# Kernel tuning notes

Hardware: AMD Instinct MI355X
Metric: run time of the kernel (lower is better)

## Reference

```python
import jax, jax.numpy as jnp
import numpy as np

P = 16           # patch size
E = P * P        # embed dim of MHA (must equal dim)
NH = 4           # num heads
HD = E // NH     # head dim


def setup_inputs() -> dict:
    key = jax.random.key(0)
    k1, k2, k3, k4, k5 = jax.random.split(key, 5)
    B, C, H, W = 2, 256, 256, 256
    scale = 1.0 / np.sqrt(E)
    return {
        "x": jax.random.normal(k1, (B, C, H, W), dtype=jnp.float32),
        "w_in": jax.random.normal(k2, (3 * E, E), dtype=jnp.float32) * scale,
        "b_in": jnp.zeros((3 * E,), dtype=jnp.float32),
        "w_out": jax.random.normal(k3, (E, E), dtype=jnp.float32) * scale,
        "b_out": jnp.zeros((E,), dtype=jnp.float32),
    }


def reference(x, w_in, b_in, w_out, b_out):
    B, C, H, W = x.shape
    nP = (H // P) * (W // P)
    # x.unfold(2,p,p).unfold(3,p,p).reshape(B,C,-1,p*p)
    patches = (
        x.reshape(B, C, H // P, P, W // P, P)
        .transpose(0, 1, 2, 4, 3, 5)
        .reshape(B, C, nP, E)
    )
    # permute(0,2,1,3).reshape(B*nP, C, p*p): batch=B*nP, seq=C, embed=E
    t = patches.transpose(0, 2, 1, 3).reshape(B * nP, C, E)

    qkv = t @ w_in.T + b_in                      # (N, C, 3E)
    q, k, v = jnp.split(qkv, 3, axis=-1)

    def to_heads(a):  # (N, C, E) -> (N, NH, C, HD)
        return a.reshape(B * nP, C, NH, HD).transpose(0, 2, 1, 3)

    q, k, v = to_heads(q), to_heads(k), to_heads(v)
    scores = jnp.einsum("nhqd,nhkd->nhqk", q * (HD ** -0.5), k)
    attn = jax.nn.softmax(scores, axis=-1)
    o = jnp.einsum("nhqk,nhkd->nhqd", attn, v)   # (N, NH, C, HD)
    o = o.transpose(0, 2, 1, 3).reshape(B * nP, C, E)
    o = o @ w_out.T + b_out
    # reshape(B, -1, C, p*p).permute(0, 2, 1, 3)
    return o.reshape(B, nP, C, E).transpose(0, 2, 1, 3)
```

## Files before the change

### kernel.cpp

```cpp
#include <hip/hip_runtime.h>
#include <hip/hip_bf16.h>

typedef __attribute__((ext_vector_type(8))) short s16x8;
typedef __attribute__((ext_vector_type(4))) float f32x4;

#define WS_SEG 67108864ULL

#if defined(__has_attribute)
#if __has_attribute(amdgpu_num_vgpr)
#define VGPR_CAP_128 __attribute__((amdgpu_num_vgpr(128)))
#else
#define VGPR_CAP_128
#endif
#else
#define VGPR_CAP_128
#endif

static __device__ __forceinline__ unsigned short f2bf(float f) {
    return __builtin_bit_cast(unsigned short, __float2bfloat16(f));
}
static __device__ __forceinline__ unsigned int pack2(float a, float b) {
    return (unsigned int)f2bf(a) | ((unsigned int)f2bf(b) << 16);
}
static __device__ __forceinline__ s16x8 u4cast(uint4 u) {
    return __builtin_bit_cast(s16x8, u);
}
static __device__ __forceinline__ void gl_lds16(const void* g, void* l) {
    __builtin_amdgcn_global_load_lds(
        (const __attribute__((address_space(1))) unsigned int*)g,
        (__attribute__((address_space(3))) unsigned int*)l, 16, 0, 0);
}

__global__ __launch_bounds__(256) void convw_swz(const float* __restrict__ wi,
                                                 unsigned short* __restrict__ wb) {
    int i = (blockIdx.x * 256 + threadIdx.x) * 4;
    float4 v = *reinterpret_cast<const float4*>(wi + i);
    int bb = i * 2;
    int row = i >> 8;
    int dst = (bb & ~127) | ((bb & 127) ^ ((row & 7) << 4));
    uint2 o = { pack2(v.x, v.y), pack2(v.z, v.w) };
    *reinterpret_cast<uint2*>((char*)wb + dst) = o;
}

__global__ __launch_bounds__(256) void gather_swz(const float* __restrict__ x,
                                                  unsigned short* __restrict__ t) {
    int q = (blockIdx.x * 256 + threadIdx.x) * 4;
    int e = q & 255, c = (q >> 8) & 255, n = q >> 16;
    int b = n >> 8, p = n & 255;
    int xi = ((b * 256 + c) * 256 + (p >> 4) * 16 + (e >> 4)) * 256 + (p & 15) * 16 + (e & 15);
    float4 v = *reinterpret_cast<const float4*>(x + xi);
    int bb = q * 2;
    int row = q >> 8;
    int dst = (bb & ~127) | ((bb & 127) ^ ((row & 7) << 4));
    uint2 o = { pack2(v.x, v.y), pack2(v.z, v.w) };
    *reinterpret_cast<uint2*>((char*)t + dst) = o;
}

template<int MODE>
__global__ __launch_bounds__(256) void gemm8(
    const unsigned short* __restrict__ Ab,
    const unsigned short* __restrict__ Wb,
    const float* __restrict__ bias,
    unsigned short* __restrict__ Qo, unsigned short* __restrict__ Ko,
    unsigned short* __restrict__ Vt, float* __restrict__ Out)
{
    __shared__ __align__(16) char smem[65536];
    char* AsB = smem;
    char* BsB = smem + 32768;

    const int t = threadIdx.x, w = t >> 6, lane = t & 63;
    const int lr = lane & 15, lk = lane >> 4;
    const int wm = w >> 1, wn = w & 1;

    constexpr int NB = (MODE == 0) ? 6 : 2;
    const int flat = blockIdx.x;
    const int xcd = flat & 7, idx = flat >> 3;
    const int bm = xcd * 128 + idx / NB;
    const int bn = idx % NB;

    const char* Ag = (const char*)Ab + (size_t)bm * 65536;
    const char* Bg = (const char*)Wb + (size_t)bn * 65536;

    const bool swapped = (MODE == 1) || (bn < 4);

    auto stage = [&](int kk) {
        char* Ad = AsB + (kk & 1) * 16384;
        char* Bd = BsB + (kk & 1) * 16384;
        #pragma unroll
        for (int i = 0; i < 4; ++i) {
            int u = (i * 4 + w) * 64 + lane;
            int row = u >> 3, cb = (u & 7) * 16;
            gl_lds16(Ag + row * 512 + kk * 128 + cb, Ad + (i * 4 + w) * 1024);
            gl_lds16(Bg + row * 512 + kk * 128 + cb, Bd + (i * 4 + w) * 1024);
        }
    };

    f32x4 acc[4][4] = {};

    stage(0);
    for (int kk = 0; kk < 4; ++kk) {
        __syncthreads();
        if (kk < 3) stage(kk + 1);
        const char* Ac = AsB + (kk & 1) * 16384;
        const char* Bc = BsB + (kk & 1) * 16384;
        #pragma unroll
        for (int kc = 0; kc < 2; ++kc) {
            s16x8 af[4], bf[4];
            #pragma unroll
            for (int fm = 0; fm < 4; ++fm) {
                int r = wm * 64 + fm * 16 + lr;
                af[fm] = *reinterpret_cast<const s16x8*>(
                    Ac + r * 128 + ((kc * 64 + lk * 16) ^ ((r & 7) << 4)));
            }
            #pragma unroll
            for (int fn = 0; fn < 4; ++fn) {
                int cc = wn * 64 + fn * 16 + lr;
                bf[fn] = *reinterpret_cast<const s16x8*>(
                    Bc + cc * 128 + ((kc * 64 + lk * 16) ^ ((cc & 7) << 4)));
            }
            if (swapped) {
                #pragma unroll
                for (int fm = 0; fm < 4; ++fm)
                    #pragma unroll
                    for (int fn = 0; fn < 4; ++fn)
                        acc[fm][fn] = __builtin_amdgcn_mfma_f32_16x16x32_bf16(bf[fn], af[fm], acc[fm][fn], 0, 0, 0);
            } else {
                #pragma unroll
                for (int fm = 0; fm < 4; ++fm)
                    #pragma unroll
                    for (int fn = 0; fn < 4; ++fn)
                        acc[fm][fn] = __builtin_amdgcn_mfma_f32_16x16x32_bf16(af[fm], bf[fn], acc[fm][fn], 0, 0, 0);
            }
        }
    }

    const int n = bm >> 1;

    if (MODE == 0) {
        if (bn < 4) {
            unsigned short* base = (bn >> 1) ? Ko : Qo;
            const int h0 = (bn & 1) * 2;
            const float qs = (bn >> 1) ? 1.0f : 0.18033688011112042f;
            #pragma unroll
            for (int fn = 0; fn < 4; ++fn) {
                int col_local = wn * 64 + fn * 16 + lk * 4;
                f32x4 bv4 = *reinterpret_cast<const f32x4*>(bias + bn * 128 + col_local);
                int h = h0 + (col_local >> 6), d0 = col_local & 63;
                #pragma unroll
                for (int fm = 0; fm < 4; ++fm) {
                    int c = (bm & 1) * 128 + wm * 64 + fm * 16 + lr;
                    uint2 st = { pack2((acc[fm][fn][0] + bv4[0]) * qs, (acc[fm][fn][1] + bv4[1]) * qs),
                                 pack2((acc[fm][fn][2] + bv4[2]) * qs, (acc[fm][fn][3] + bv4[3]) * qs) };
                    *reinterpret_cast<uint2*>(
                        (char*)base + (size_t)((n * 4 + h) * 256 + c) * 128 + d0 * 2) = st;
                }
            }
        } else {
            const int h0 = (bn - 4) * 2;
            #pragma unroll
            for (int fn = 0; fn < 4; ++fn) {
                int col_local = wn * 64 + fn * 16 + lr;
                float bv = bias[bn * 128 + col_local];
                int hl = col_local >> 6, d = col_local & 63;
                #pragma unroll
                for (int fm = 0; fm < 4; ++fm) {
                    int c = (bm & 1) * 128 + wm * 64 + fm * 16 + lk * 4;
                    uint2 st = { pack2(acc[fm][fn][0] + bv, acc[fm][fn][1] + bv),
                                 pack2(acc[fm][fn][2] + bv, acc[fm][fn][3] + bv) };
                    *reinterpret_cast<uint2*>(
                        (char*)Vt + (size_t)((n * 4 + h0 + hl) * 64 + d) * 512 + c * 2) = st;
                }
            }
        }
    } else {
        #pragma unroll
        for (int fn = 0; fn < 4; ++fn) {
            int colg = bn * 128 + wn * 64 + fn * 16 + lk * 4;
            f32x4 bv4 = *reinterpret_cast<const f32x4*>(bias + colg);
            #pragma unroll
            for (int fm = 0; fm < 4; ++fm) {
                int rg = bm * 128 + wm * 64 + fm * 16 + lr;
                int nn = rg >> 8, c = rg & 255;
                int b = nn >> 8, p = nn & 255;
                f32x4 st = acc[fm][fn] + bv4;
                *reinterpret_cast<f32x4*>(
                    Out + (((size_t)(b * 256 + c) * 256 + p) << 8) + colg) = st;
            }
        }
    }
}

__global__ __launch_bounds__(1024) VGPR_CAP_128 void attn8(
    const unsigned short* __restrict__ Q,
    const unsigned short* __restrict__ K,
    const unsigned short* __restrict__ V,
    unsigned short* __restrict__ O)
{
    __shared__ __align__(16) char KsB[32768];
    __shared__ __align__(16) char VsB[32768];

    const int nh = blockIdx.x;
    const int n = nh >> 2, h = nh & 3;
    const int t = threadIdx.x, w = t >> 6, lane = t & 63;
    const int lr = lane & 15, lk = lane >> 4;

    const unsigned short* Qg = Q + (size_t)nh * 16384;
    const char* Kg = (const char*)K + (size_t)nh * 32768;
    const char* Vg = (const char*)V + (size_t)nh * 32768;

    #pragma unroll
    for (int i = 0; i < 2; ++i) {
        int u = i * 1024 + t;
        int row = u >> 3, cb = (u & 7) * 16;
        uint4 val = *reinterpret_cast<const uint4*>(Kg + u * 16);
        *reinterpret_cast<uint4*>(KsB + row * 128 + (cb ^ ((row & 7) << 4))) = val;
    }
    #pragma unroll
    for (int i = 0; i < 2; ++i) {
        int u = i * 1024 + t;
        int row = u >> 5, cb = (u & 31) * 16;
        uint4 val = *reinterpret_cast<const uint4*>(Vg + u * 16);
        *reinterpret_cast<uint4*>(VsB + row * 512 + (cb ^ ((row & 7) << 4))) = val;
    }
    __syncthreads();

    const int swz = (lr & 7) << 4;
    const int qt = w;

    s16x8 bq0 = *reinterpret_cast<const s16x8*>(Qg + (qt * 16 + lr) * 64 + lk * 8);
    s16x8 bq1 = *reinterpret_cast<const s16x8*>(Qg + (qt * 16 + lr) * 64 + 32 + lk * 8);

    f32x4 oacc[4] = {};
    float l = 0.f;

    #pragma unroll
    for (int kb = 0; kb < 8; ++kb) {
        const int rb0 = ((2 * kb) * 16 + lr) * 128;
        const int rb1 = ((2 * kb + 1) * 16 + lr) * 128;
        s16x8 a00 = *reinterpret_cast<const s16x8*>(KsB + rb0 + ((lk * 16) ^ swz));
        s16x8 a01 = *reinterpret_cast<const s16x8*>(KsB + rb0 + ((64 + lk * 16) ^ swz));
        s16x8 a10 = *reinterpret_cast<const s16x8*>(KsB + rb1 + ((lk * 16) ^ swz));
        s16x8 a11 = *reinterpret_cast<const s16x8*>(KsB + rb1 + ((64 + lk * 16) ^ swz));
        f32x4 s0 = { 0.f, 0.f, 0.f, 0.f }, s1 = { 0.f, 0.f, 0.f, 0.f };
        __builtin_amdgcn_s_setprio(1);
        s0 = __builtin_amdgcn_mfma_f32_16x16x32_bf16(a00, bq0, s0, 0, 0, 0);
        s0 = __builtin_amdgcn_mfma_f32_16x16x32_bf16(a01, bq1, s0, 0, 0, 0);
        s1 = __builtin_amdgcn_mfma_f32_16x16x32_bf16(a10, bq0, s1, 0, 0, 0);
        s1 = __builtin_amdgcn_mfma_f32_16x16x32_bf16(a11, bq1, s1, 0, 0, 0);
        __builtin_amdgcn_s_setprio(0);

        float p0 = exp2f(s0[0]), p1 = exp2f(s0[1]);
        float p2 = exp2f(s0[2]), p3 = exp2f(s0[3]);
        float p4 = exp2f(s1[0]), p5 = exp2f(s1[1]);
        float p6 = exp2f(s1[2]), p7 = exp2f(s1[3]);
        l += ((p0 + p1) + (p2 + p3)) + ((p4 + p5) + (p6 + p7));
        uint4 pk = { pack2(p0, p1), pack2(p2, p3), pack2(p4, p5), pack2(p6, p7) };
        s16x8 pf = u4cast(pk);

        __builtin_amdgcn_s_setprio(1);
        #pragma unroll
        for (int dt = 0; dt < 4; ++dt) {
            const char* vb = VsB + (dt * 16 + lr) * 512;
            uint2 v0 = *reinterpret_cast<const uint2*>(vb + ((kb * 64 + lk * 8) ^ swz));
            uint2 v1 = *reinterpret_cast<const uint2*>(vb + ((kb * 64 + lk * 8 + 32) ^ swz));
            uint4 uu = { v0.x, v0.y, v1.x, v1.y };
            oacc[dt] = __builtin_amdgcn_mfma_f32_16x16x32_bf16(u4cast(uu), pf, oacc[dt], 0, 0, 0);
        }
        __builtin_amdgcn_s_setprio(0);
    }

    l += __shfl_xor(l, 16);
    l += __shfl_xor(l, 32);
    const float rl = 1.0f / l;

    char* orow = (char*)O + (size_t)(n * 256 + qt * 16 + lr) * 512 + h * 128;
    #pragma unroll
    for (int dt = 0; dt < 4; ++dt) {
        uint2 st = { pack2(oacc[dt][0] * rl, oacc[dt][1] * rl),
                     pack2(oacc[dt][2] * rl, oacc[dt][3] * rl) };
        *reinterpret_cast<uint2*>(orow + ((dt * 32 + lk * 8) ^ swz)) = st;
    }
}

extern "C" void kernel_launch(void* const* d_in, const int* in_sizes, int n_in,
                              void* d_out, int out_size, void* d_ws, size_t ws_size,
                              hipStream_t stream) {
    const float* x     = (const float*)d_in[0];
    const float* w_in  = (const float*)d_in[1];
    const float* b_in  = (const float*)d_in[2];
    const float* w_out = (const float*)d_in[3];
    const float* b_out = (const float*)d_in[4];

    char* ws = (char*)d_ws;
    unsigned short* tO = (unsigned short*)(ws);
    unsigned short* Qw = (unsigned short*)(ws + WS_SEG);
    unsigned short* Kw = (unsigned short*)(ws + 2 * WS_SEG);
    unsigned short* Vw = (unsigned short*)(ws + 3 * WS_SEG);

    unsigned short* WbIn = (unsigned short*)((float*)d_out + out_size - 98304);

    convw_swz<<<192, 256, 0, stream>>>(w_in, WbIn);
    gather_swz<<<32768, 256, 0, stream>>>(x, tO);

    gemm8<0><<<6144, 256, 0, stream>>>(tO, WbIn, b_in, Qw, Kw, Vw, nullptr);

    attn8<<<2048, 1024, 0, stream>>>(Qw, Kw, Vw, tO);

    unsigned short* WbOut = Kw;
    convw_swz<<<64, 256, 0, stream>>>(w_out, WbOut);

    gemm8<1><<<2048, 256, 0, stream>>>(tO, WbOut, b_out,
                                       nullptr, nullptr, nullptr, (float*)d_out);
}
```

Baseline: 289.2 us.

## Fuse patch gather into QKV projection GEMM with fragment-packed weights

```diff
diff --git a/kernel.cpp b/kernel.cpp
--- a/kernel.cpp
+++ b/kernel.cpp
@@ -31,6 +31,21 @@
         (__attribute__((address_space(3))) unsigned int*)l, 16, 0, 0);
 }
 
+__global__ __launch_bounds__(256) void convw_frag(const float* __restrict__ wi,
+                                                  unsigned short* __restrict__ wp) {
+    int o8 = blockIdx.x * 256 + threadIdx.x;
+    int nkc = o8 >> 10;
+    int rem = o8 & 1023;
+    int row = rem >> 2;
+    int lk8 = (rem & 3) * 8;
+    int Ni = nkc >> 3, kk = (nkc >> 1) & 3, kc = nkc & 1;
+    const float* src = wi + ((size_t)(Ni * 256 + row)) * 256 + kk * 64 + kc * 32 + lk8;
+    float4 a = *reinterpret_cast<const float4*>(src);
+    float4 b = *reinterpret_cast<const float4*>(src + 4);
+    uint4 o = { pack2(a.x, a.y), pack2(a.z, a.w), pack2(b.x, b.y), pack2(b.z, b.w) };
+    *reinterpret_cast<uint4*>(wp + o8 * 8) = o;
+}
+
 __global__ __launch_bounds__(256) void convw_swz(const float* __restrict__ wi,
                                                  unsigned short* __restrict__ wb) {
     int i = (blockIdx.x * 256 + threadIdx.x) * 4;
@@ -42,27 +57,126 @@
     *reinterpret_cast<uint2*>((char*)wb + dst) = o;
 }
 
-__global__ __launch_bounds__(256) void gather_swz(const float* __restrict__ x,
-                                                  unsigned short* __restrict__ t) {
-    int q = (blockIdx.x * 256 + threadIdx.x) * 4;
-    int e = q & 255, c = (q >> 8) & 255, n = q >> 16;
-    int b = n >> 8, p = n & 255;
-    int xi = ((b * 256 + c) * 256 + (p >> 4) * 16 + (e >> 4)) * 256 + (p & 15) * 16 + (e & 15);
-    float4 v = *reinterpret_cast<const float4*>(x + xi);
-    int bb = q * 2;
-    int row = q >> 8;
-    int dst = (bb & ~127) | ((bb & 127) ^ ((row & 7) << 4));
-    uint2 o = { pack2(v.x, v.y), pack2(v.z, v.w) };
-    *reinterpret_cast<uint2*>((char*)t + dst) = o;
-}
-
-template<int MODE>
-__global__ __launch_bounds__(256) void gemm8(
+__global__ __launch_bounds__(512) void qkv_fused(
+    const float* __restrict__ Xf,
+    const unsigned short* __restrict__ Wp,
+    const float* __restrict__ bias,
+    unsigned short* __restrict__ Qo, unsigned short* __restrict__ Ko,
+    unsigned short* __restrict__ Vt)
+{
+    __shared__ __align__(16) char AsB[131072];
+
+    const int t = threadIdx.x, w = t >> 6, lane = t & 63;
+    const int lr = lane & 15, lk = lane >> 4;
+    const int wm = w >> 2, wn = w & 3;
+
+    const int bid = blockIdx.x;
+    const int b = bid >> 8, pp = (bid >> 1) & 127, ch = bid & 1;
+    const int p16 = pp >> 3, col0 = (pp & 7) * 32;
+    const int c0 = ch * 128;
+
+    {
+        const float* xb = Xf + ((size_t)(b * 256 + c0) * 256 + p16 * 16) * 256 + col0;
+        #pragma unroll
+        for (int j = 0; j < 16; ++j) {
+            int u = j * 512 + t;
+            int c = u >> 6;
+            int r = (u >> 2) & 15;
+            int cf8 = (u & 3) * 8;
+            const float* p = xb + ((size_t)c * 256 + r) * 256 + cf8;
+            float4 a = *reinterpret_cast<const float4*>(p);
+            float4 b4 = *reinterpret_cast<const float4*>(p + 4);
+            int m = ((cf8 >> 4) << 7) + c;
+            int within = (r & 3) * 32 + (cf8 & 15) * 2;
+            int addr = m * 512 + (r >> 2) * 128 + (within ^ ((m & 7) << 4));
+            uint4 o = { pack2(a.x, a.y), pack2(a.z, a.w),
+                        pack2(b4.x, b4.y), pack2(b4.z, b4.w) };
+            *reinterpret_cast<uint4*>(AsB + addr) = o;
+        }
+    }
+    __syncthreads();
+
+    const int n = b * 256 + pp * 2 + wm;
+
+    #pragma unroll
+    for (int Ni = 0; Ni < 3; ++Ni) {
+        f32x4 acc[8][4] = {};
+        #pragma unroll
+        for (int kk = 0; kk < 4; ++kk) {
+            #pragma unroll
+            for (int kc = 0; kc < 2; ++kc) {
+                const char* wbase = (const char*)Wp + (((Ni * 4 + kk) * 2 + kc) << 14);
+                s16x8 bfr[4];
+                #pragma unroll
+                for (int fn = 0; fn < 4; ++fn)
+                    bfr[fn] = *reinterpret_cast<const s16x8*>(
+                        wbase + ((wn * 64 + fn * 16 + lr) * 32 + lk * 8) * 2);
+                const int e2 = kk * 128 + kc * 64 + lk * 16;
+                const int cbase = e2 & ~127, within = e2 & 127;
+                s16x8 afr[8];
+                #pragma unroll
+                for (int fm = 0; fm < 8; ++fm) {
+                    int m = wm * 128 + fm * 16 + lr;
+                    afr[fm] = *reinterpret_cast<const s16x8*>(
+                        AsB + m * 512 + cbase + (within ^ ((m & 7) << 4)));
+                }
+                if (Ni < 2) {
+                    #pragma unroll
+                    for (int fm = 0; fm < 8; ++fm)
+                        #pragma unroll
+                        for (int fn = 0; fn < 4; ++fn)
+                            acc[fm][fn] = __builtin_amdgcn_mfma_f32_16x16x32_bf16(bfr[fn], afr[fm], acc[fm][fn], 0, 0, 0);
+                } else {
+                    #pragma unroll
+                    for (int fm = 0; fm < 8; ++fm)
+                        #pragma unroll
+                        for (int fn = 0; fn < 4; ++fn)
+                            acc[fm][fn] = __builtin_amdgcn_mfma_f32_16x16x32_bf16(afr[fm], bfr[fn], acc[fm][fn], 0, 0, 0);
+                }
+            }
+        }
+
+        if (Ni < 2) {
+            unsigned short* base = Ni ? Ko : Qo;
+            const float qs = Ni ? 1.0f : 0.18033688011112042f;
+            #pragma unroll
+            for (int fn = 0; fn < 4; ++fn) {
+                int colq = wn * 64 + fn * 16 + lk * 4;
+                f32x4 bv4 = *reinterpret_cast<const f32x4*>(bias + Ni * 256 + colq);
+                int h = colq >> 6, d0 = colq & 63;
+                #pragma unroll
+                for (int fm = 0; fm < 8; ++fm) {
+                    int c = c0 + fm * 16 + lr;
+                    uint2 st = { pack2((acc[fm][fn][0] + bv4[0]) * qs, (acc[fm][fn][1] + bv4[1]) * qs),
+                                 pack2((acc[fm][fn][2] + bv4[2]) * qs, (acc[fm][fn][3] + bv4[3]) * qs) };
+                    *reinterpret_cast<uint2*>(
+                        (char*)base + (size_t)((n * 4 + h) * 256 + c) * 128 + d0 * 2) = st;
+                }
+            }
+        } else {
+            #pragma unroll
+            for (int fn = 0; fn < 4; ++fn) {
+                int dcol = wn * 64 + fn * 16 + lr;
+                float bv = bias[512 + dcol];
+                int h = dcol >> 6, d = dcol & 63;
+                #pragma unroll
+                for (int fm = 0; fm < 8; ++fm) {
+                    int c = c0 + fm * 16 + lk * 4;
+                    uint2 st = { pack2(acc[fm][fn][0] + bv, acc[fm][fn][1] + bv),
+                                 pack2(acc[fm][fn][2] + bv, acc[fm][fn][3] + bv) };
+                    *reinterpret_cast<uint2*>(
+                        (char*)Vt + (size_t)((n * 4 + h) * 64 + d) * 512 + c * 2) = st;
+                }
+            }
+        }
+    }
+}
+
+__global__ __launch_bounds__(256) void gemm_out(
     const unsigned short* __restrict__ Ab,
     const unsigned short* __restrict__ Wb,
     const float* __restrict__ bias,
-    unsigned short* __restrict__ Qo, unsigned short* __restrict__ Ko,
-    unsigned short* __restrict__ Vt, float* __restrict__ Out)
+    float* __restrict__ Out)
 {
     __shared__ __align__(16) char smem[65536];
     char* AsB = smem;
@@ -72,16 +186,13 @@
     const int lr = lane & 15, lk = lane >> 4;
     const int wm = w >> 1, wn = w & 1;
 
-    constexpr int NB = (MODE == 0) ? 6 : 2;
     const int flat = blockIdx.x;
     const int xcd = flat & 7, idx = flat >> 3;
-    const int bm = xcd * 128 + idx / NB;
-    const int bn = idx % NB;
+    const int bm = xcd * 128 + idx / 2;
+    const int bn = idx % 2;
 
     const char* Ag = (const char*)Ab + (size_t)bm * 65536;
     const char* Bg = (const char*)Wb + (size_t)bn * 65536;
-
-    const bool swapped = (MODE == 1) || (bn < 4);
 
     auto stage = [&](int kk) {
         char* Ad = AsB + (kk & 1) * 16384;
@@ -118,74 +229,26 @@
                 bf[fn] = *reinterpret_cast<const s16x8*>(
                     Bc + cc * 128 + ((kc * 64 + lk * 16) ^ ((cc & 7) << 4)));
             }
-            if (swapped) {
-                #pragma unroll
-                for (int fm = 0; fm < 4; ++fm)
-                    #pragma unroll
-                    for (int fn = 0; fn < 4; ++fn)
-                        acc[fm][fn] = __builtin_amdgcn_mfma_f32_16x16x32_bf16(bf[fn], af[fm], acc[fm][fn], 0, 0, 0);
-            } else {
-                #pragma unroll
-                for (int fm = 0; fm < 4; ++fm)
-                    #pragma unroll
-                    for (int fn = 0; fn < 4; ++fn)
-                        acc[fm][fn] = __builtin_amdgcn_mfma_f32_16x16x32_bf16(af[fm], bf[fn], acc[fm][fn], 0, 0, 0);
-            }
-        }
-    }
-
-    const int n = bm >> 1;
-
-    if (MODE == 0) {
-        if (bn < 4) {
-            unsigned short* base = (bn >> 1) ? Ko : Qo;
-            const int h0 = (bn & 1) * 2;
-            const float qs = (bn >> 1) ? 1.0f : 0.18033688011112042f;
-            #pragma unroll
-            for (int fn = 0; fn < 4; ++fn) {
-                int col_local = wn * 64 + fn * 16 + lk * 4;
-                f32x4 bv4 = *reinterpret_cast<const f32x4*>(bias + bn * 128 + col_local);
-                int h = h0 + (col_local >> 6), d0 = col_local & 63;
-                #pragma unroll
-                for (int fm = 0; fm < 4; ++fm) {
-                    int c = (bm & 1) * 128 + wm * 64 + fm * 16 + lr;
-                    uint2 st = { pack2((acc[fm][fn][0] + bv4[0]) * qs, (acc[fm][fn][1] + bv4[1]) * qs),
-                                 pack2((acc[fm][fn][2] + bv4[2]) * qs, (acc[fm][fn][3] + bv4[3]) * qs) };
-                    *reinterpret_cast<uint2*>(
-                        (char*)base + (size_t)((n * 4 + h) * 256 + c) * 128 + d0 * 2) = st;
-                }
-            }
-        } else {
-            const int h0 = (bn - 4) * 2;
-            #pragma unroll
-            for (int fn = 0; fn < 4; ++fn) {
-                int col_local = wn * 64 + fn * 16 + lr;
-                float bv = bias[bn * 128 + col_local];
-                int hl = col_local >> 6, d = col_local & 63;
-                #pragma unroll
-                for (int fm = 0; fm < 4; ++fm) {
-                    int c = (bm & 1) * 128 + wm * 64 + fm * 16 + lk * 4;
-                    uint2 st = { pack2(acc[fm][fn][0] + bv, acc[fm][fn][1] + bv),
-                                 pack2(acc[fm][fn][2] + bv, acc[fm][fn][3] + bv) };
-                    *reinterpret_cast<uint2*>(
-                        (char*)Vt + (size_t)((n * 4 + h0 + hl) * 64 + d) * 512 + c * 2) = st;
-                }
-            }
-        }
-    } else {
-        #pragma unroll
-        for (int fn = 0; fn < 4; ++fn) {
-            int colg = bn * 128 + wn * 64 + fn * 16 + lk * 4;
-            f32x4 bv4 = *reinterpret_cast<const f32x4*>(bias + colg);
-            #pragma unroll
-            for (int fm = 0; fm < 4; ++fm) {
-                int rg = bm * 128 + wm * 64 + fm * 16 + lr;
-                int nn = rg >> 8, c = rg & 255;
-                int b = nn >> 8, p = nn & 255;
-                f32x4 st = acc[fm][fn] + bv4;
-                *reinterpret_cast<f32x4*>(
-                    Out + (((size_t)(b * 256 + c) * 256 + p) << 8) + colg) = st;
-            }
+            #pragma unroll
+            for (int fm = 0; fm < 4; ++fm)
+                #pragma unroll
+                for (int fn = 0; fn < 4; ++fn)
+                    acc[fm][fn] = __builtin_amdgcn_mfma_f32_16x16x32_bf16(bf[fn], af[fm], acc[fm][fn], 0, 0, 0);
+        }
+    }
+
+    #pragma unroll
+    for (int fn = 0; fn < 4; ++fn) {
+        int colg = bn * 128 + wn * 64 + fn * 16 + lk * 4;
+        f32x4 bv4 = *reinterpret_cast<const f32x4*>(bias + colg);
+        #pragma unroll
+        for (int fm = 0; fm < 4; ++fm) {
+            int rg = bm * 128 + wm * 64 + fm * 16 + lr;
+            int nn = rg >> 8, c = rg & 255;
+            int b = nn >> 8, p = nn & 255;
+            f32x4 st = acc[fm][fn] + bv4;
+            *reinterpret_cast<f32x4*>(
+                Out + (((size_t)(b * 256 + c) * 256 + p) << 8) + colg) = st;
         }
     }
 }
@@ -299,16 +362,14 @@
 
     unsigned short* WbIn = (unsigned short*)((float*)d_out + out_size - 98304);
 
-    convw_swz<<<192, 256, 0, stream>>>(w_in, WbIn);
-    gather_swz<<<32768, 256, 0, stream>>>(x, tO);
-
-    gemm8<0><<<6144, 256, 0, stream>>>(tO, WbIn, b_in, Qw, Kw, Vw, nullptr);
+    convw_frag<<<96, 256, 0, stream>>>(w_in, WbIn);
+
+    qkv_fused<<<512, 512, 0, stream>>>(x, WbIn, b_in, Qw, Kw, Vw);
 
     attn8<<<2048, 1024, 0, stream>>>(Qw, Kw, Vw, tO);
 
     unsigned short* WbOut = Kw;
     convw_swz<<<64, 256, 0, stream>>>(w_out, WbOut);
 
-    gemm8<1><<<2048, 256, 0, stream>>>(tO, WbOut, b_out,
-                                       nullptr, nullptr, nullptr, (float*)d_out);
-}
+    gemm_out<<<2048, 256, 0, stream>>>(tO, WbOut, b_out, (float*)d_out);
+}
```

Measured after the change: 292.4 us. Within noise of the previous version (+1.1%).

## Widen GEMM tiles to 128x256 and read pre-fragmented weights straight from global

Applied to the files above, without the earlier changes.

```diff
diff --git a/kernel.cpp b/kernel.cpp
--- a/kernel.cpp
+++ b/kernel.cpp
@@ -31,15 +31,19 @@
         (__attribute__((address_space(3))) unsigned int*)l, 16, 0, 0);
 }
 
-__global__ __launch_bounds__(256) void convw_swz(const float* __restrict__ wi,
-                                                 unsigned short* __restrict__ wb) {
-    int i = (blockIdx.x * 256 + threadIdx.x) * 4;
-    float4 v = *reinterpret_cast<const float4*>(wi + i);
-    int bb = i * 2;
-    int row = i >> 8;
-    int dst = (bb & ~127) | ((bb & 127) ^ ((row & 7) << 4));
-    uint2 o = { pack2(v.x, v.y), pack2(v.z, v.w) };
-    *reinterpret_cast<uint2*>((char*)wb + dst) = o;
+__global__ __launch_bounds__(256) void convw_frag(const float* __restrict__ wi,
+                                                  unsigned short* __restrict__ wp) {
+    int o8 = blockIdx.x * 256 + threadIdx.x;
+    int nkc = o8 >> 10;
+    int rem = o8 & 1023;
+    int row = rem >> 2;
+    int lk8 = (rem & 3) * 8;
+    int Ni = nkc >> 3, kk = (nkc >> 1) & 3, kc = nkc & 1;
+    const float* src = wi + ((size_t)(Ni * 256 + row)) * 256 + kk * 64 + kc * 32 + lk8;
+    float4 a = *reinterpret_cast<const float4*>(src);
+    float4 b = *reinterpret_cast<const float4*>(src + 4);
+    uint4 o = { pack2(a.x, a.y), pack2(a.z, a.w), pack2(b.x, b.y), pack2(b.z, b.w) };
+    *reinterpret_cast<uint4*>(wp + o8 * 8) = o;
 }
 
 __global__ __launch_bounds__(256) void gather_swz(const float* __restrict__ x,
@@ -57,79 +61,71 @@
 }
 
 template<int MODE>
-__global__ __launch_bounds__(256) void gemm8(
+__global__ __launch_bounds__(512) void gemm10(
     const unsigned short* __restrict__ Ab,
-    const unsigned short* __restrict__ Wb,
+    const unsigned short* __restrict__ Wp,
     const float* __restrict__ bias,
     unsigned short* __restrict__ Qo, unsigned short* __restrict__ Ko,
     unsigned short* __restrict__ Vt, float* __restrict__ Out)
 {
-    __shared__ __align__(16) char smem[65536];
-    char* AsB = smem;
-    char* BsB = smem + 32768;
+    __shared__ __align__(16) char AsB[32768];
 
     const int t = threadIdx.x, w = t >> 6, lane = t & 63;
     const int lr = lane & 15, lk = lane >> 4;
-    const int wm = w >> 1, wn = w & 1;
-
-    constexpr int NB = (MODE == 0) ? 6 : 2;
+    const int wm = w >> 2, wn = w & 3;
+
+    constexpr int NB = (MODE == 0) ? 3 : 1;
     const int flat = blockIdx.x;
     const int xcd = flat & 7, idx = flat >> 3;
     const int bm = xcd * 128 + idx / NB;
     const int bn = idx % NB;
 
     const char* Ag = (const char*)Ab + (size_t)bm * 65536;
-    const char* Bg = (const char*)Wb + (size_t)bn * 65536;
-
-    const bool swapped = (MODE == 1) || (bn < 4);
-
-    auto stage = [&](int kk) {
+
+    auto stageA = [&](int kk) {
         char* Ad = AsB + (kk & 1) * 16384;
-        char* Bd = BsB + (kk & 1) * 16384;
         #pragma unroll
-        for (int i = 0; i < 4; ++i) {
-            int u = (i * 4 + w) * 64 + lane;
+        for (int i = 0; i < 2; ++i) {
+            int u = i * 512 + t;
             int row = u >> 3, cb = (u & 7) * 16;
-            gl_lds16(Ag + row * 512 + kk * 128 + cb, Ad + (i * 4 + w) * 1024);
-            gl_lds16(Bg + row * 512 + kk * 128 + cb, Bd + (i * 4 + w) * 1024);
+            gl_lds16(Ag + row * 512 + kk * 128 + cb, Ad + (i * 8 + w) * 1024);
         }
     };
 
     f32x4 acc[4][4] = {};
 
-    stage(0);
+    stageA(0);
     for (int kk = 0; kk < 4; ++kk) {
         __syncthreads();
-        if (kk < 3) stage(kk + 1);
+        if (kk < 3) stageA(kk + 1);
         const char* Ac = AsB + (kk & 1) * 16384;
-        const char* Bc = BsB + (kk & 1) * 16384;
         #pragma unroll
         for (int kc = 0; kc < 2; ++kc) {
-            s16x8 af[4], bf[4];
+            const char* wb = (const char*)Wp + (((bn * 4 + kk) * 2 + kc) << 14);
+            s16x8 bfr[4];
+            #pragma unroll
+            for (int fn = 0; fn < 4; ++fn)
+                bfr[fn] = *reinterpret_cast<const s16x8*>(
+                    wb + ((wn * 64 + fn * 16 + lr) * 32 + lk * 8) * 2);
+            s16x8 af[4];
             #pragma unroll
             for (int fm = 0; fm < 4; ++fm) {
                 int r = wm * 64 + fm * 16 + lr;
                 af[fm] = *reinterpret_cast<const s16x8*>(
                     Ac + r * 128 + ((kc * 64 + lk * 16) ^ ((r & 7) << 4)));
             }
-            #pragma unroll
-            for (int fn = 0; fn < 4; ++fn) {
-                int cc = wn * 64 + fn * 16 + lr;
-                bf[fn] = *reinterpret_cast<const s16x8*>(
-                    Bc + cc * 128 + ((kc * 64 + lk * 16) ^ ((cc & 7) << 4)));
-            }
-            if (swapped) {
+            if (MODE == 1 || bn < 2) {
                 #pragma unroll
                 for (int fm = 0; fm < 4; ++fm)
                     #pragma unroll
                     for (int fn = 0; fn < 4; ++fn)
-                        acc[fm][fn] = __builtin_amdgcn_mfma_f32_16x16x32_bf16(bf[fn], af[fm], acc[fm][fn], 0, 0, 0);
+                        acc[fm][fn] = __builtin_amdgcn_mfma_f32_16x16x32_bf16(bfr[fn], af[fm], acc[fm][fn], 0, 0, 0);
             } else {
                 #pragma unroll
                 for (int fm = 0; fm < 4; ++fm)
                     #pragma unroll
                     for (int fn = 0; fn < 4; ++fn)
-                        acc[fm][fn] = __builtin_amdgcn_mfma_f32_16x16x32_bf16(af[fm], bf[fn], acc[fm][fn], 0, 0, 0);
+                        acc[fm][fn] = __builtin_amdgcn_mfma_f32_16x16x32_bf16(af[fm], bfr[fn], acc[fm][fn], 0, 0, 0);
             }
         }
     }
@@ -137,15 +133,14 @@
     const int n = bm >> 1;
 
     if (MODE == 0) {
-        if (bn < 4) {
-            unsigned short* base = (bn >> 1) ? Ko : Qo;
-            const int h0 = (bn & 1) * 2;
-            const float qs = (bn >> 1) ? 1.0f : 0.18033688011112042f;
+        if (bn < 2) {
+            unsigned short* base = bn ? Ko : Qo;
+            const float qs = bn ? 1.0f : 0.18033688011112042f;
             #pragma unroll
             for (int fn = 0; fn < 4; ++fn) {
-                int col_local = wn * 64 + fn * 16 + lk * 4;
-                f32x4 bv4 = *reinterpret_cast<const f32x4*>(bias + bn * 128 + col_local);
-                int h = h0 + (col_local >> 6), d0 = col_local & 63;
+                int col = wn * 64 + fn * 16 + lk * 4;
+                f32x4 bv4 = *reinterpret_cast<const f32x4*>(bias + bn * 256 + col);
+                int h = col >> 6, d0 = col & 63;
                 #pragma unroll
                 for (int fm = 0; fm < 4; ++fm) {
                     int c = (bm & 1) * 128 + wm * 64 + fm * 16 + lr;
@@ -156,26 +151,25 @@
                 }
             }
         } else {
-            const int h0 = (bn - 4) * 2;
             #pragma unroll
             for (int fn = 0; fn < 4; ++fn) {
-                int col_local = wn * 64 + fn * 16 + lr;
-                float bv = bias[bn * 128 + col_local];
-                int hl = col_local >> 6, d = col_local & 63;
+                int dcol = wn * 64 + fn * 16 + lr;
+                float bv = bias[512 + dcol];
+                int h = dcol >> 6, d = dcol & 63;
                 #pragma unroll
                 for (int fm = 0; fm < 4; ++fm) {
                     int c = (bm & 1) * 128 + wm * 64 + fm * 16 + lk * 4;
                     uint2 st = { pack2(acc[fm][fn][0] + bv, acc[fm][fn][1] + bv),
                                  pack2(acc[fm][fn][2] + bv, acc[fm][fn][3] + bv) };
                     *reinterpret_cast<uint2*>(
-                        (char*)Vt + (size_t)((n * 4 + h0 + hl) * 64 + d) * 512 + c * 2) = st;
+                        (char*)Vt + (size_t)((n * 4 + h) * 64 + d) * 512 + c * 2) = st;
                 }
             }
         }
     } else {
         #pragma unroll
         for (int fn = 0; fn < 4; ++fn) {
-            int colg = bn * 128 + wn * 64 + fn * 16 + lk * 4;
+            int colg = wn * 64 + fn * 16 + lk * 4;
             f32x4 bv4 = *reinterpret_cast<const f32x4*>(bias + colg);
             #pragma unroll
             for (int fm = 0; fm < 4; ++fm) {
@@ -299,16 +293,16 @@
 
     unsigned short* WbIn = (unsigned short*)((float*)d_out + out_size - 98304);
 
-    convw_swz<<<192, 256, 0, stream>>>(w_in, WbIn);
+    convw_frag<<<96, 256, 0, stream>>>(w_in, WbIn);
     gather_swz<<<32768, 256, 0, stream>>>(x, tO);
 
-    gemm8<0><<<6144, 256, 0, stream>>>(tO, WbIn, b_in, Qw, Kw, Vw, nullptr);
+    gemm10<0><<<3072, 512, 0, stream>>>(tO, WbIn, b_in, Qw, Kw, Vw, nullptr);
 
     attn8<<<2048, 1024, 0, stream>>>(Qw, Kw, Vw, tO);
 
     unsigned short* WbOut = Kw;
-    convw_swz<<<64, 256, 0, stream>>>(w_out, WbOut);
-
-    gemm8<1><<<2048, 256, 0, stream>>>(tO, WbOut, b_out,
-                                       nullptr, nullptr, nullptr, (float*)d_out);
-}
+    convw_frag<<<32, 256, 0, stream>>>(w_out, WbOut);
+
+    gemm10<1><<<1024, 512, 0, stream>>>(tO, WbOut, b_out,
+                                        nullptr, nullptr, nullptr, (float*)d_out);
+}
```

Result: slower. 314.0 us (+8.6%).
